# Optimization experiments

Measured on AMD Instinct MI355X. Metric: run time of the kernel, lower is better.

Reference implementation:

```python
import jax, jax.numpy as jnp
import numpy as np

BS, NC, BH, BW, C = 1, 6, 100, 100, 256
HG, WG = 100, 40
HF, WF = 48, 80
HEADS, PTS, HD = 8, 8, 32
MAXOV = 2
NQ = HG * WG


def _nearest_sample(img, grid):
    # img: [B,H,W,Ch], grid: [B,Hg,Wg,2] in [-1,1]; nearest, align_corners=True, zeros padding
    B, H, W, _ = img.shape
    ix = jnp.round((grid[..., 0] + 1.0) * 0.5 * (W - 1))
    iy = jnp.round((grid[..., 1] + 1.0) * 0.5 * (H - 1))
    valid = (ix >= 0) & (ix <= W - 1) & (iy >= 0) & (iy <= H - 1)
    xc = jnp.clip(ix, 0, W - 1).astype(jnp.int32)
    yc = jnp.clip(iy, 0, H - 1).astype(jnp.int32)
    b = jnp.arange(B)[:, None, None]
    return img[b, yc, xc] * valid[..., None]


def _bilinear_sample(img, x, y):
    # img: [B,H,W,Ch]; x,y: [B,N] unnormalized (align_corners=False); zeros padding
    B, H, W, _ = img.shape
    x0 = jnp.floor(x)
    y0 = jnp.floor(y)
    wx1 = x - x0
    wy1 = y - y0
    b = jnp.arange(B)[:, None]

    def corner(xi, yi):
        valid = (xi >= 0) & (xi <= W - 1) & (yi >= 0) & (yi <= H - 1)
        xc = jnp.clip(xi, 0, W - 1).astype(jnp.int32)
        yc = jnp.clip(yi, 0, H - 1).astype(jnp.int32)
        return img[b, yc, xc] * valid[..., None]

    return (corner(x0, y0) * ((1 - wx1) * (1 - wy1))[..., None]
            + corner(x0 + 1, y0) * (wx1 * (1 - wy1))[..., None]
            + corner(x0, y0 + 1) * ((1 - wx1) * wy1)[..., None]
            + corner(x0 + 1, y0 + 1) * (wx1 * wy1)[..., None])


def _forward(query, value, queries_rebatch_grid, restore_bev_grid,
             reference_points_rebatch, bev_pillar_counts, query_pos,
             Wv, bv, Woff, boff, Watt, batt, Wout, bout, spatial_shapes):
    inp_residual = query
    q = query + query_pos                                       # [BS, BH*BW, C]
    # --- rebatch BEV queries per camera via nearest grid_sample ---
    qmap = jnp.broadcast_to(q.reshape(BS, 1, BH, BW, C),
                            (BS, NC, BH, BW, C)).reshape(BS * NC, BH, BW, C)
    q_reb = _nearest_sample(qmap, queries_rebatch_grid).reshape(BS * NC, NQ, C)
    ref = reference_points_rebatch.reshape(BS * NC, NQ, 2)      # flatten(-2): [BNC,NQ,2,1]->[BNC,NQ,2]
    # --- value projection ---
    v = value.transpose(2, 0, 1, 3).reshape(BS * NC, HF * WF, C)
    v = (v @ Wv + bv).reshape(BS * NC, HF, WF, HEADS, HD)
    # --- multi-scale deformable attention (single level) ---
    off = (q_reb @ Woff + boff).reshape(BS * NC, NQ, HEADS, PTS, 2)
    attw = jax.nn.softmax((q_reb @ Watt + batt).reshape(BS * NC, NQ, HEADS, PTS), axis=-1)
    normalizer = jnp.flip(spatial_shapes[0], 0).astype(jnp.float32)  # [WF, HF]
    loc = ref[:, :, None, None, :] + off / normalizer           # [BNC,NQ,HEADS,PTS,2] in [0,1]
    x = (loc[..., 0] * WF - 0.5).transpose(0, 2, 1, 3).reshape(BS * NC * HEADS, NQ * PTS)
    y = (loc[..., 1] * HF - 0.5).transpose(0, 2, 1, 3).reshape(BS * NC * HEADS, NQ * PTS)
    vh = v.transpose(0, 3, 1, 2, 4).reshape(BS * NC * HEADS, HF, WF, HD)
    samp = _bilinear_sample(vh, x, y).reshape(BS * NC, HEADS, NQ, PTS, HD)
    out = jnp.einsum('bhnpd,bnhp->bnhd', samp, attw).reshape(BS * NC, NQ, C)
    queries_out = out.transpose(0, 2, 1)                        # [BNC, C, NQ] (channels-first as module expects)
    # --- restore to BEV feature ---
    qo = queries_out.reshape(BS, NC, C, NQ).transpose(0, 2, 1, 3).reshape(BS, C, NC * HG, WG)
    bevq = _nearest_sample(qo.transpose(0, 2, 3, 1), restore_bev_grid)  # [BS, MAXOV*BH, BW, C]
    bevq = bevq.transpose(0, 3, 1, 2)                           # [BS, C, MAXOV*BH, BW]
    # reshape(BS, C*MAXOV, BH, BW) + all-ones grouped 1x1 conv == sum of the two overlap copies
    slots = bevq[:, :, :BH, :] + bevq[:, :, BH:, :]             # [BS, C, BH, BW]
    slots = slots.reshape(BS, C, BH * BW).transpose(0, 2, 1)    # [BS, BH*BW, C]
    slots = slots * bev_pillar_counts
    slots = slots @ Wout + bout
    return slots + inp_residual  # dropout identity in eval


def setup_inputs():
    key = jax.random.key(0)
    ks = jax.random.split(key, 14)
    s = 1.0 / np.sqrt(C)
    return {
        "query": jax.random.normal(ks[0], (BS, BH * BW, C), jnp.float32),
        "value": jax.random.normal(ks[1], (BS, HF * WF, NC, C), jnp.float32),
        "queries_rebatch_grid": jax.random.uniform(ks[2], (BS * NC, HG, WG, 2), jnp.float32, -1.0, 1.0),
        "restore_bev_grid": jax.random.uniform(ks[3], (BS, MAXOV * BH, BW, 2), jnp.float32, -1.0, 1.0),
        "reference_points_rebatch": jax.random.uniform(ks[4], (BS * NC, NQ, 2, 1), jnp.float32),
        "bev_pillar_counts": jax.random.uniform(ks[5], (BS, BH * BW, 1), jnp.float32),
        "query_pos": jax.random.normal(ks[6], (BS, BH * BW, C), jnp.float32),
        "Wv": jax.random.uniform(ks[7], (C, C), jnp.float32, -s, s),
        "bv": jnp.zeros((C,), jnp.float32),
        "Woff": jax.random.normal(ks[8], (C, HEADS * PTS * 2), jnp.float32) * 0.01,
        "boff": jax.random.uniform(ks[9], (HEADS * PTS * 2,), jnp.float32, -2.0, 2.0),
        "Watt": jax.random.normal(ks[10], (C, HEADS * PTS), jnp.float32) * 0.01,
        "batt": jnp.zeros((HEADS * PTS,), jnp.float32),
        "Wout": jax.random.uniform(ks[11], (C, C), jnp.float32, -s, s),
        "bout": jnp.zeros((C,), jnp.float32),
        "spatial_shapes": jnp.array([[HF, WF]], dtype=jnp.int32),
    }


def reference(query, value, queries_rebatch_grid, restore_bev_grid,
              reference_points_rebatch, bev_pillar_counts, query_pos,
              Wv, bv, Woff, boff, Watt, batt, Wout, bout, spatial_shapes):
    return _forward(query, value, queries_rebatch_grid, restore_bev_grid,
                    reference_points_rebatch, bev_pillar_counts, query_pos,
                    Wv, bv, Woff, boff, Watt, batt, Wout, bout, spatial_shapes)
```

## Files before the change

### kernel.cpp

```cpp
#include <hip/hip_runtime.h>
#include <hip/hip_bf16.h>
#include <math.h>

#define NCAMS 6
#define BH_ 100
#define BW_ 100
#define CDIM 256
#define NQ_ 4000
#define HF_ 48
#define WF_ 80
#define HEADS_ 8
#define PTS_ 8
#define HD_ 32
#define HWV (HF_*WF_)
#define M1_ (NCAMS*HWV)
#define M2_ (NCAMS*NQ_)
#define NOUT_ 10000

#define SA 264
#define SOFF 132
#define SATT 68

typedef __bf16 bf16_t;
typedef __bf16 bf16x8 __attribute__((ext_vector_type(8)));
typedef __bf16 bf16x4 __attribute__((ext_vector_type(4)));
typedef float  f32x4  __attribute__((ext_vector_type(4)));

static __device__ __forceinline__ f32x4 mfma16(bf16x8 a, bf16x8 b, f32x4 c) {
    return __builtin_amdgcn_mfma_f32_16x16x32_bf16(a, b, c, 0, 0, 0);
}

__global__ __launch_bounds__(256) void k0_prep(const float* __restrict__ Wv,
                                               const float* __restrict__ Woff,
                                               const float* __restrict__ Watt,
                                               const float* __restrict__ Wout,
                                               bf16_t* __restrict__ WvT,
                                               bf16_t* __restrict__ WcombT,
                                               bf16_t* __restrict__ WoutT) {
    int b = blockIdx.x, k = threadIdx.x;
    if (b < 256) {
        WvT[b * 256 + k] = (bf16_t)Wv[k * 256 + b];
    } else if (b < 448) {
        int n = b - 256;
        float v = (n < 128) ? Woff[k * 128 + n] : Watt[k * 64 + (n - 128)];
        WcombT[n * 256 + k] = (bf16_t)v;
    } else {
        int n = b - 448;
        WoutT[n * 256 + k] = (bf16_t)Wout[k * 256 + n];
    }
}

__global__ __launch_bounds__(256) void k1_vproj(const float* __restrict__ value,
                                                const bf16_t* __restrict__ WvT,
                                                const float* __restrict__ bv,
                                                bf16_t* __restrict__ vh) {
    __shared__ __align__(16) bf16_t At[32 * SA];
    const int m0 = blockIdx.x * 32;
    const int cam = m0 / HWV;
    const int hw0 = m0 - cam * HWV;
    for (int idx = threadIdx.x; idx < 32 * 64; idx += 256) {
        int r = idx >> 6, c4 = idx & 63;
        float4 v = ((const float4*)value)[((hw0 + r) * NCAMS + cam) * 64 + c4];
        bf16x4 pk; pk[0] = (bf16_t)v.x; pk[1] = (bf16_t)v.y; pk[2] = (bf16_t)v.z; pk[3] = (bf16_t)v.w;
        *(bf16x4*)(At + r * SA + c4 * 4) = pk;
    }
    __syncthreads();
    const int lane = threadIdx.x & 63, w = threadIdx.x >> 6;
    const int lr = lane & 15, lk = lane >> 4;
    f32x4 acc[2][4] = {};
    const bf16_t* a0 = At + lr * SA + lk * 8;
    const bf16_t* b0 = WvT + (w * 64 + lr) * 256 + lk * 8;
#pragma unroll
    for (int ks = 0; ks < 8; ++ks) {
        bf16x8 af[2], bf_[4];
#pragma unroll
        for (int mm = 0; mm < 2; ++mm) af[mm] = *(const bf16x8*)(a0 + mm * 16 * SA + ks * 32);
#pragma unroll
        for (int n = 0; n < 4; ++n) bf_[n] = *(const bf16x8*)(b0 + n * 16 * 256 + ks * 32);
#pragma unroll
        for (int mm = 0; mm < 2; ++mm)
#pragma unroll
            for (int n = 0; n < 4; ++n)
                acc[mm][n] = mfma16(af[mm], bf_[n], acc[mm][n]);
    }
    __syncthreads();
#pragma unroll
    for (int n = 0; n < 4; ++n) {
        int col = w * 64 + n * 16 + lr;
        float bias = bv[col];
#pragma unroll
        for (int mm = 0; mm < 2; ++mm)
#pragma unroll
            for (int j = 0; j < 4; ++j)
                At[(mm * 16 + lk * 4 + j) * SA + col] = (bf16_t)(acc[mm][n][j] + bias);
    }
    __syncthreads();
    for (int idx = threadIdx.x; idx < 32 * 32; idx += 256) {
        int r = idx >> 5, g = idx & 31;
        int head = g >> 2, part = g & 3;
        bf16x8 v = *(const bf16x8*)(At + r * SA + g * 8);
        *(bf16x8*)(vh + ((size_t)(cam * HEADS_ + head) * HWV + hw0 + r) * HD_ + part * 8) = v;
    }
}

__global__ __launch_bounds__(256) void k23_offatt_sample(
        const float* __restrict__ query,
        const float* __restrict__ qpos,
        const float* __restrict__ qgrid,
        const bf16_t* __restrict__ WcombT,
        const float* __restrict__ boff,
        const float* __restrict__ batt,
        const float* __restrict__ refp,
        const bf16_t* __restrict__ vh,
        bf16_t* __restrict__ out_attn) {
    __shared__ __align__(16) char u_lds[16 * SOFF * 4 + 16 * SATT * 4];
    bf16_t* At   = (bf16_t*)u_lds;
    float*  offs = (float*)u_lds;
    float*  atts = (float*)(u_lds + 16 * SOFF * 4);
    __shared__ int rowpos[16];
    __shared__ float rref[16][2];

    const int orig = blockIdx.x;
    const int xcd = orig & 7, idx8 = orig >> 3;
    const int lb = (xcd < 4 ? xcd * 188 : 4 * 188 + (xcd - 4) * 187) + idx8;
    const int m0 = lb * 16;
    const int cam = m0 / NQ_;

    if (threadIdx.x < 16) {
        int m = m0 + threadIdx.x;
        float gx = qgrid[m * 2 + 0], gy = qgrid[m * 2 + 1];
        float fx = rintf(__fmul_rn(__fmul_rn(__fadd_rn(gx, 1.0f), 0.5f), 99.0f));
        float fy = rintf(__fmul_rn(__fmul_rn(__fadd_rn(gy, 1.0f), 0.5f), 99.0f));
        bool valid = (fx >= 0.0f) && (fx <= 99.0f) && (fy >= 0.0f) && (fy <= 99.0f);
        rowpos[threadIdx.x] = valid ? ((int)fy * BW_ + (int)fx) : -1;
    } else if (threadIdx.x < 48) {
        int t = threadIdx.x - 16;
        rref[t >> 1][t & 1] = refp[(m0 + (t >> 1)) * 2 + (t & 1)];
    }
    __syncthreads();
    const float4* q4 = (const float4*)query;
    const float4* p4 = (const float4*)qpos;
    {
        int idx = threadIdx.x;
#pragma unroll
        for (int it = 0; it < 4; ++it, idx += 256) {
            int r = idx >> 6, c4 = idx & 63;
            int p = rowpos[r];
            bf16x4 pk;
            if (p >= 0) {
                float4 a = q4[p * 64 + c4];
                float4 b = p4[p * 64 + c4];
                pk[0] = (bf16_t)(a.x + b.x); pk[1] = (bf16_t)(a.y + b.y);
                pk[2] = (bf16_t)(a.z + b.z); pk[3] = (bf16_t)(a.w + b.w);
            } else {
                pk[0] = (bf16_t)0.0f; pk[1] = (bf16_t)0.0f; pk[2] = (bf16_t)0.0f; pk[3] = (bf16_t)0.0f;
            }
            *(bf16x4*)(At + r * SA + c4 * 4) = pk;
        }
    }
    __syncthreads();
    const int lane = threadIdx.x & 63, w = threadIdx.x >> 6;
    const int lr = lane & 15, lk = lane >> 4;
    const int wcol0 = w * 48;
    f32x4 acc[3] = {};
    {
        const bf16_t* a0 = At + lr * SA + lk * 8;
        const bf16_t* b0 = WcombT + (wcol0 + lr) * 256 + lk * 8;
#pragma unroll
        for (int ks = 0; ks < 8; ++ks) {
            bf16x8 af = *(const bf16x8*)(a0 + ks * 32);
            bf16x8 bf_[3];
#pragma unroll
            for (int n = 0; n < 3; ++n) bf_[n] = *(const bf16x8*)(b0 + n * 16 * 256 + ks * 32);
#pragma unroll
            for (int n = 0; n < 3; ++n)
                acc[n] = mfma16(af, bf_[n], acc[n]);
        }
    }
    __syncthreads();
#pragma unroll
    for (int n = 0; n < 3; ++n) {
        const int colbase = wcol0 + n * 16;
        const int col = colbase + lr;
        const int rloc = lk * 4;
        if (colbase < 128) {
            float bo = boff[col];
#pragma unroll
            for (int j = 0; j < 4; ++j)
                offs[(rloc + j) * SOFF + col] = acc[n][j] + bo;
        } else {
            float bt = batt[col - 128];
#pragma unroll
            for (int j = 0; j < 4; ++j) {
                float lg = acc[n][j] + bt;
                float mx = lg;
                mx = fmaxf(mx, __shfl_xor(mx, 1, 64));
                mx = fmaxf(mx, __shfl_xor(mx, 2, 64));
                mx = fmaxf(mx, __shfl_xor(mx, 4, 64));
                float e = expf(lg - mx);
                float s = e;
                s += __shfl_xor(s, 1, 64);
                s += __shfl_xor(s, 2, 64);
                s += __shfl_xor(s, 4, 64);
                atts[(rloc + j) * SATT + (col - 128)] = e / s;
            }
        }
    }
    __syncthreads();
    const int j = threadIdx.x & 3;
#pragma unroll
    for (int rep = 0; rep < 2; ++rep) {
        const int unit = rep * 64 + (threadIdx.x >> 2);
        const int r = unit >> 3, h = unit & 7;
        const int m = m0 + r;
        const float rx = rref[r][0];
        const float ry = rref[r][1];
        const bf16_t* base = vh + (size_t)(cam * HEADS_ + h) * HWV * HD_ + j * 8;
        const float4* off4 = (const float4*)(offs + r * SOFF + h * 16);
        const float4* att4 = (const float4*)(atts + r * SATT + h * 8);
        float4 o0 = off4[0], o1 = off4[1], o2 = off4[2], o3 = off4[3];
        float4 a0 = att4[0], a1 = att4[1];
        float offv[16] = {o0.x, o0.y, o0.z, o0.w, o1.x, o1.y, o1.z, o1.w,
                          o2.x, o2.y, o2.z, o2.w, o3.x, o3.y, o3.z, o3.w};
        float attv[8] = {a0.x, a0.y, a0.z, a0.w, a1.x, a1.y, a1.z, a1.w};
        float acc2[8] = {};
#pragma unroll
        for (int p = 0; p < PTS_; ++p) {
            float ax = fmaf(rx, (float)WF_, offv[p * 2 + 0] - 0.5f);
            float ay = fmaf(ry, (float)HF_, offv[p * 2 + 1] - 0.5f);
            float x0f = floorf(ax), y0f = floorf(ay);
            float wx = ax - x0f, wy = ay - y0f;
            float att = attv[p];
            bool vx0 = (x0f >= 0.0f) && (x0f <= (float)(WF_ - 1));
            bool vx1 = (x0f >= -1.0f) && (x0f <= (float)(WF_ - 2));
            bool vy0 = (y0f >= 0.0f) && (y0f <= (float)(HF_ - 1));
            bool vy1 = (y0f >= -1.0f) && (y0f <= (float)(HF_ - 2));
            float aw00 = (vx0 && vy0) ? att * (1.0f - wx) * (1.0f - wy) : 0.0f;
            float aw01 = (vx1 && vy0) ? att * wx * (1.0f - wy) : 0.0f;
            float aw10 = (vx0 && vy1) ? att * (1.0f - wx) * wy : 0.0f;
            float aw11 = (vx1 && vy1) ? att * wx * wy : 0.0f;
            int x0 = (int)fminf(fmaxf(x0f, 0.0f), (float)(WF_ - 1));
            int x1 = (int)fminf(fmaxf(x0f + 1.0f, 0.0f), (float)(WF_ - 1));
            int y0 = (int)fminf(fmaxf(y0f, 0.0f), (float)(HF_ - 1));
            int y1 = (int)fminf(fmaxf(y0f + 1.0f, 0.0f), (float)(HF_ - 1));
            bf16x8 c00 = *(const bf16x8*)(base + (y0 * WF_ + x0) * HD_);
            bf16x8 c01 = *(const bf16x8*)(base + (y0 * WF_ + x1) * HD_);
            bf16x8 c10 = *(const bf16x8*)(base + (y1 * WF_ + x0) * HD_);
            bf16x8 c11 = *(const bf16x8*)(base + (y1 * WF_ + x1) * HD_);
#pragma unroll
            for (int c = 0; c < 8; ++c) {
                acc2[c] = fmaf(aw00, (float)c00[c],
                          fmaf(aw01, (float)c01[c],
                          fmaf(aw10, (float)c10[c],
                          fmaf(aw11, (float)c11[c], acc2[c]))));
            }
        }
        bf16x8 ov;
#pragma unroll
        for (int c = 0; c < 8; ++c) ov[c] = (bf16_t)acc2[c];
        *(bf16x8*)(out_attn + (size_t)m * CDIM + h * HD_ + j * 8) = ov;
    }
}

__global__ __launch_bounds__(256) void k4_restore(const bf16_t* __restrict__ out_attn,
                                                  const float* __restrict__ rgrid,
                                                  const float* __restrict__ counts,
                                                  const bf16_t* __restrict__ WoutT,
                                                  const float* __restrict__ bout,
                                                  const float* __restrict__ query,
                                                  float* __restrict__ out) {
    __shared__ __align__(16) bf16_t At[32 * SA];
    __shared__ int pos2[32][2];
    __shared__ float cnt[32];
    const int m0 = blockIdx.x * 32;
    if (threadIdx.x < 64) {
        int r = threadIdx.x >> 1, k = threadIdx.x & 1;
        int i = m0 + r;
        if (i < NOUT_) {
            int bh = i / 100, bw = i - bh * 100;
            int R = bh + k * BH_;
            float gx = rgrid[(R * 100 + bw) * 2 + 0], gy = rgrid[(R * 100 + bw) * 2 + 1];
            float fx = rintf(__fmul_rn(__fmul_rn(__fadd_rn(gx, 1.0f), 0.5f), 39.0f));
            float fy = rintf(__fmul_rn(__fmul_rn(__fadd_rn(gy, 1.0f), 0.5f), 599.0f));
            bool valid = (fx >= 0.0f) && (fx <= 39.0f) && (fy >= 0.0f) && (fy <= 599.0f);
            int ix = (int)fx, iy = (int)fy;
            int camr = iy / 100, hg = iy - camr * 100;
            pos2[r][k] = valid ? (camr * NQ_ + hg * 40 + ix) : -1;
            if (k == 0) cnt[r] = counts[i];
        } else {
            pos2[r][k] = -1;
            if (k == 0) cnt[r] = 0.0f;
        }
    }
    __syncthreads();
    for (int idx = threadIdx.x; idx < 32 * 32; idx += 256) {
        int r = idx >> 5, g = idx & 31;
        int p0 = pos2[r][0], p1 = pos2[r][1];
        float s[8] = {};
        if (p0 >= 0) {
            bf16x8 a = *(const bf16x8*)(out_attn + (size_t)p0 * CDIM + g * 8);
#pragma unroll
            for (int c = 0; c < 8; ++c) s[c] += (float)a[c];
        }
        if (p1 >= 0) {
            bf16x8 a = *(const bf16x8*)(out_attn + (size_t)p1 * CDIM + g * 8);
#pragma unroll
            for (int c = 0; c < 8; ++c) s[c] += (float)a[c];
        }
        float cn = cnt[r];
        bf16x8 pk;
#pragma unroll
        for (int c = 0; c < 8; ++c) pk[c] = (bf16_t)(s[c] * cn);
        *(bf16x8*)(At + r * SA + g * 8) = pk;
    }
    __syncthreads();
    const int lane = threadIdx.x & 63, w = threadIdx.x >> 6;
    const int lr = lane & 15, lk = lane >> 4;
    f32x4 acc[2][4] = {};
    const bf16_t* a0 = At + lr * SA + lk * 8;
    const bf16_t* b0 = WoutT + (w * 64 + lr) * 256 + lk * 8;
#pragma unroll
    for (int ks = 0; ks < 8; ++ks) {
        bf16x8 af[2], bf_[4];
#pragma unroll
        for (int mm = 0; mm < 2; ++mm) af[mm] = *(const bf16x8*)(a0 + mm * 16 * SA + ks * 32);
#pragma unroll
        for (int n = 0; n < 4; ++n) bf_[n] = *(const bf16x8*)(b0 + n * 16 * 256 + ks * 32);
#pragma unroll
        for (int mm = 0; mm < 2; ++mm)
#pragma unroll
            for (int n = 0; n < 4; ++n)
                acc[mm][n] = mfma16(af[mm], bf_[n], acc[mm][n]);
    }
#pragma unroll
    for (int n = 0; n < 4; ++n) {
        int col = w * 64 + n * 16 + lr;
        float bo = bout[col];
#pragma unroll
        for (int mm = 0; mm < 2; ++mm)
#pragma unroll
            for (int j = 0; j < 4; ++j) {
                int row = m0 + mm * 16 + lk * 4 + j;
                if (row < NOUT_)
                    out[row * CDIM + col] = acc[mm][n][j] + bo + query[row * CDIM + col];
            }
    }
}

extern "C" void kernel_launch(void* const* d_in, const int* in_sizes, int n_in,
                              void* d_out, int out_size, void* d_ws, size_t ws_size,
                              hipStream_t stream) {
    (void)in_sizes; (void)n_in; (void)out_size; (void)ws_size;
    const float* query  = (const float*)d_in[0];
    const float* value  = (const float*)d_in[1];
    const float* qgrid  = (const float*)d_in[2];
    const float* rgrid  = (const float*)d_in[3];
    const float* refp   = (const float*)d_in[4];
    const float* counts = (const float*)d_in[5];
    const float* qpos   = (const float*)d_in[6];
    const float* Wv     = (const float*)d_in[7];
    const float* bv     = (const float*)d_in[8];
    const float* Woff   = (const float*)d_in[9];
    const float* boff   = (const float*)d_in[10];
    const float* Watt   = (const float*)d_in[11];
    const float* batt   = (const float*)d_in[12];
    const float* Wout   = (const float*)d_in[13];
    const float* bout   = (const float*)d_in[14];
    float* out = (float*)d_out;
    char* w8 = (char*)d_ws;

    bf16_t* vh       = (bf16_t*)(w8);
    bf16_t* out_attn = (bf16_t*)(w8 + 11796480);
    bf16_t* WvT      = (bf16_t*)(w8 + 24084480);
    bf16_t* WcombT   = (bf16_t*)(w8 + 24215552);
    bf16_t* WoutT    = (bf16_t*)(w8 + 24313856);

    hipLaunchKernelGGL(k0_prep,   dim3(704),      dim3(256), 0, stream, Wv, Woff, Watt, Wout,
                       WvT, WcombT, WoutT);
    hipLaunchKernelGGL(k1_vproj,  dim3(M1_ / 32), dim3(256), 0, stream, value, WvT, bv, vh);
    hipLaunchKernelGGL(k23_offatt_sample, dim3(M2_ / 16), dim3(256), 0, stream,
                       query, qpos, qgrid, WcombT, boff, batt, refp, vh, out_attn);
    hipLaunchKernelGGL(k4_restore, dim3(313),     dim3(256), 0, stream, out_attn, rgrid, counts,
                       WoutT, bout, query, out);
}
```

Baseline: 95.25 us.

## Store shifted duplicate value map and precompute bf16 query sum

The value projection now writes a second copy of the per-head value map, shifted by one pixel, so each pair of horizontally adjacent bilinear corners sits in one contiguous 128-byte span. The sampler splits each head across 8 lanes instead of 4, issues two wide loads per point instead of four, and combines the x-halves with a shuffle. The query+pos sum is precomputed once in bf16 in the prep kernel, which cuts the gather traffic in the sampling kernel. In exchange, value-map memory and write traffic double and the prep kernel gains extra blocks.

```diff
diff --git a/kernel.cpp b/kernel.cpp
--- a/kernel.cpp
+++ b/kernel.cpp
@@ -16,6 +16,7 @@
 #define M1_ (NCAMS*HWV)
 #define M2_ (NCAMS*NQ_)
 #define NOUT_ 10000
+#define VHSHIFT 5898240
 
 #define SA 264
 #define SOFF 132
@@ -34,9 +35,12 @@
                                                const float* __restrict__ Woff,
                                                const float* __restrict__ Watt,
                                                const float* __restrict__ Wout,
+                                               const float* __restrict__ query,
+                                               const float* __restrict__ qpos,
                                                bf16_t* __restrict__ WvT,
                                                bf16_t* __restrict__ WcombT,
-                                               bf16_t* __restrict__ WoutT) {
+                                               bf16_t* __restrict__ WoutT,
+                                               bf16_t* __restrict__ qsum) {
     int b = blockIdx.x, k = threadIdx.x;
     if (b < 256) {
         WvT[b * 256 + k] = (bf16_t)Wv[k * 256 + b];
@@ -44,9 +48,19 @@
         int n = b - 256;
         float v = (n < 128) ? Woff[k * 128 + n] : Watt[k * 64 + (n - 128)];
         WcombT[n * 256 + k] = (bf16_t)v;
-    } else {
+    } else if (b < 704) {
         int n = b - 448;
         WoutT[n * 256 + k] = (bf16_t)Wout[k * 256 + n];
+    } else {
+        int row0 = (b - 704) * 4;
+        int r = k >> 6, c4 = k & 63;
+        int i = (row0 + r) * 64 + c4;
+        float4 a = ((const float4*)query)[i];
+        float4 p = ((const float4*)qpos)[i];
+        bf16x4 pk;
+        pk[0] = (bf16_t)(a.x + p.x); pk[1] = (bf16_t)(a.y + p.y);
+        pk[2] = (bf16_t)(a.z + p.z); pk[3] = (bf16_t)(a.w + p.w);
+        *(bf16x4*)(qsum + (size_t)i * 4) = pk;
     }
 }
 
@@ -99,13 +113,19 @@
         int r = idx >> 5, g = idx & 31;
         int head = g >> 2, part = g & 3;
         bf16x8 v = *(const bf16x8*)(At + r * SA + g * 8);
-        *(bf16x8*)(vh + ((size_t)(cam * HEADS_ + head) * HWV + hw0 + r) * HD_ + part * 8) = v;
+        int hw = hw0 + r;
+        int y = hw / WF_;
+        int x = hw - y * WF_;
+        size_t rowbase = ((size_t)(cam * HEADS_ + head) * HF_ + y) * (WF_ * HD_);
+        int o = x * HD_ + part * 8;
+        *(bf16x8*)(vh + rowbase + o) = v;
+        if (o >= 32) *(bf16x8*)(vh + VHSHIFT + rowbase + o - 32) = v;
+        if (x == WF_ - 1) *(bf16x8*)(vh + VHSHIFT + rowbase + o) = v;
     }
 }
 
 __global__ __launch_bounds__(256) void k23_offatt_sample(
-        const float* __restrict__ query,
-        const float* __restrict__ qpos,
+        const bf16_t* __restrict__ qsum,
         const float* __restrict__ qgrid,
         const bf16_t* __restrict__ WcombT,
         const float* __restrict__ boff,
@@ -138,24 +158,16 @@
         rref[t >> 1][t & 1] = refp[(m0 + (t >> 1)) * 2 + (t & 1)];
     }
     __syncthreads();
-    const float4* q4 = (const float4*)query;
-    const float4* p4 = (const float4*)qpos;
     {
         int idx = threadIdx.x;
 #pragma unroll
-        for (int it = 0; it < 4; ++it, idx += 256) {
-            int r = idx >> 6, c4 = idx & 63;
+        for (int it = 0; it < 2; ++it, idx += 256) {
+            int r = idx >> 5, g = idx & 31;
             int p = rowpos[r];
-            bf16x4 pk;
-            if (p >= 0) {
-                float4 a = q4[p * 64 + c4];
-                float4 b = p4[p * 64 + c4];
-                pk[0] = (bf16_t)(a.x + b.x); pk[1] = (bf16_t)(a.y + b.y);
-                pk[2] = (bf16_t)(a.z + b.z); pk[3] = (bf16_t)(a.w + b.w);
-            } else {
-                pk[0] = (bf16_t)0.0f; pk[1] = (bf16_t)0.0f; pk[2] = (bf16_t)0.0f; pk[3] = (bf16_t)0.0f;
-            }
-            *(bf16x4*)(At + r * SA + c4 * 4) = pk;
+            bf16x8 v;
+            if (p >= 0) v = *(const bf16x8*)(qsum + (size_t)p * 256 + g * 8);
+            else { bf16x8 z = {}; v = z; }
+            *(bf16x8*)(At + r * SA + g * 8) = v;
         }
     }
     __syncthreads();
@@ -207,22 +219,25 @@
         }
     }
     __syncthreads();
-    const int j = threadIdx.x & 3;
-#pragma unroll
-    for (int rep = 0; rep < 2; ++rep) {
-        const int unit = rep * 64 + (threadIdx.x >> 2);
+    const int lane8 = threadIdx.x & 7;
+    const int jj    = lane8 & 3;
+    const int xsel  = lane8 >> 2;
+    const int uu    = threadIdx.x >> 3;
+#pragma unroll
+    for (int pass = 0; pass < 4; ++pass) {
+        const int unit = pass * 32 + uu;
         const int r = unit >> 3, h = unit & 7;
-        const int m = m0 + r;
-        const float rx = rref[r][0];
-        const float ry = rref[r][1];
-        const bf16_t* base = vh + (size_t)(cam * HEADS_ + h) * HWV * HD_ + j * 8;
+        const bf16_t* bhead = vh + (size_t)(cam * HEADS_ + h) * HWV * HD_;
+        const float rx = rref[r][0], ry = rref[r][1];
         const float4* off4 = (const float4*)(offs + r * SOFF + h * 16);
-        const float4* att4 = (const float4*)(atts + r * SATT + h * 8);
-        float4 o0 = off4[0], o1 = off4[1], o2 = off4[2], o3 = off4[3];
-        float4 a0 = att4[0], a1 = att4[1];
-        float offv[16] = {o0.x, o0.y, o0.z, o0.w, o1.x, o1.y, o1.z, o1.w,
-                          o2.x, o2.y, o2.z, o2.w, o3.x, o3.y, o3.z, o3.w};
-        float attv[8] = {a0.x, a0.y, a0.z, a0.w, a1.x, a1.y, a1.z, a1.w};
+        float offv[16];
+#pragma unroll
+        for (int q = 0; q < 4; ++q) {
+            float4 a = off4[q];
+            offv[q * 4 + 0] = a.x; offv[q * 4 + 1] = a.y;
+            offv[q * 4 + 2] = a.z; offv[q * 4 + 3] = a.w;
+        }
+        const float* attp = atts + r * SATT + h * 8;
         float acc2[8] = {};
 #pragma unroll
         for (int p = 0; p < PTS_; ++p) {
@@ -230,7 +245,7 @@
             float ay = fmaf(ry, (float)HF_, offv[p * 2 + 1] - 0.5f);
             float x0f = floorf(ax), y0f = floorf(ay);
             float wx = ax - x0f, wy = ay - y0f;
-            float att = attv[p];
+            float att = attp[p];
             bool vx0 = (x0f >= 0.0f) && (x0f <= (float)(WF_ - 1));
             bool vx1 = (x0f >= -1.0f) && (x0f <= (float)(WF_ - 2));
             bool vy0 = (y0f >= 0.0f) && (y0f <= (float)(HF_ - 1));
@@ -239,26 +254,29 @@
             float aw01 = (vx1 && vy0) ? att * wx * (1.0f - wy) : 0.0f;
             float aw10 = (vx0 && vy1) ? att * (1.0f - wx) * wy : 0.0f;
             float aw11 = (vx1 && vy1) ? att * wx * wy : 0.0f;
-            int x0 = (int)fminf(fmaxf(x0f, 0.0f), (float)(WF_ - 1));
-            int x1 = (int)fminf(fmaxf(x0f + 1.0f, 0.0f), (float)(WF_ - 1));
+            bool px = (x0f >= 0.0f);
+            float wy0 = xsel ? (px ? aw01 : 0.0f) : (px ? aw00 : aw01);
+            float wy1 = xsel ? (px ? aw11 : 0.0f) : (px ? aw10 : aw11);
+            int xs = (int)fminf(fmaxf(x0f, 0.0f), (float)(WF_ - 1));
+            int par = xs & 1;
+            int tb = xs - par;
             int y0 = (int)fminf(fmaxf(y0f, 0.0f), (float)(HF_ - 1));
             int y1 = (int)fminf(fmaxf(y0f + 1.0f, 0.0f), (float)(HF_ - 1));
-            bf16x8 c00 = *(const bf16x8*)(base + (y0 * WF_ + x0) * HD_);
-            bf16x8 c01 = *(const bf16x8*)(base + (y0 * WF_ + x1) * HD_);
-            bf16x8 c10 = *(const bf16x8*)(base + (y1 * WF_ + x0) * HD_);
-            bf16x8 c11 = *(const bf16x8*)(base + (y1 * WF_ + x1) * HD_);
-#pragma unroll
-            for (int c = 0; c < 8; ++c) {
-                acc2[c] = fmaf(aw00, (float)c00[c],
-                          fmaf(aw01, (float)c01[c],
-                          fmaf(aw10, (float)c10[c],
-                          fmaf(aw11, (float)c11[c], acc2[c]))));
-            }
+            const bf16_t* bp = bhead + (size_t)par * VHSHIFT;
+            bf16x8 e0 = *(const bf16x8*)(bp + (y0 * WF_ + tb) * HD_ + lane8 * 8);
+            bf16x8 e1 = *(const bf16x8*)(bp + (y1 * WF_ + tb) * HD_ + lane8 * 8);
+#pragma unroll
+            for (int c = 0; c < 8; ++c)
+                acc2[c] = fmaf(wy0, (float)e0[c], fmaf(wy1, (float)e1[c], acc2[c]));
         }
         bf16x8 ov;
 #pragma unroll
-        for (int c = 0; c < 8; ++c) ov[c] = (bf16_t)acc2[c];
-        *(bf16x8*)(out_attn + (size_t)m * CDIM + h * HD_ + j * 8) = ov;
+        for (int c = 0; c < 8; ++c) {
+            float tot = acc2[c] + __shfl_xor(acc2[c], 4, 64);
+            ov[c] = (bf16_t)tot;
+        }
+        if (xsel == 0)
+            *(bf16x8*)(out_attn + (size_t)(m0 + r) * CDIM + h * HD_ + jj * 8) = ov;
     }
 }
 
@@ -370,16 +388,17 @@
     char* w8 = (char*)d_ws;
 
     bf16_t* vh       = (bf16_t*)(w8);
-    bf16_t* out_attn = (bf16_t*)(w8 + 11796480);
-    bf16_t* WvT      = (bf16_t*)(w8 + 24084480);
-    bf16_t* WcombT   = (bf16_t*)(w8 + 24215552);
-    bf16_t* WoutT    = (bf16_t*)(w8 + 24313856);
-
-    hipLaunchKernelGGL(k0_prep,   dim3(704),      dim3(256), 0, stream, Wv, Woff, Watt, Wout,
-                       WvT, WcombT, WoutT);
+    bf16_t* out_attn = (bf16_t*)(w8 + 23592960);
+    bf16_t* WvT      = (bf16_t*)(w8 + 35880960);
+    bf16_t* WcombT   = (bf16_t*)(w8 + 36012032);
+    bf16_t* WoutT    = (bf16_t*)(w8 + 36110336);
+    bf16_t* qsum     = (bf16_t*)(w8 + 36241408);
+
+    hipLaunchKernelGGL(k0_prep,   dim3(3204),     dim3(256), 0, stream, Wv, Woff, Watt, Wout,
+                       query, qpos, WvT, WcombT, WoutT, qsum);
     hipLaunchKernelGGL(k1_vproj,  dim3(M1_ / 32), dim3(256), 0, stream, value, WvT, bv, vh);
     hipLaunchKernelGGL(k23_offatt_sample, dim3(M2_ / 16), dim3(256), 0, stream,
-                       query, qpos, qgrid, WcombT, boff, batt, refp, vh, out_attn);
+                       qsum, qgrid, WcombT, boff, batt, refp, vh, out_attn);
     hipLaunchKernelGGL(k4_restore, dim3(313),     dim3(256), 0, stream, out_attn, rgrid, counts,
                        WoutT, bout, query, out);
 }
```

Measured after the change: 97.73 us. +2.6%, slower.
